# Optimization experiments

Hardware: AMD Instinct MI355X
Metric: run time of the kernel (lower is better)

The kernel has to match this reference:

```python
import jax, jax.numpy as jnp
import numpy as np

# ---- static config mirroring __init__ kwargs ----
B, GH, GW = 64, 52, 52
A, NC = 5, 80            # anchor_number, class_number
HW = GH * GW
MAXB = 30                # max_box_per_image
NET_W, NET_H = 416.0, 416.0
COORD_SCALE, NOOBJ_SCALE, OBJ_SCALE, CLASS_SCALE = 5.0, 1.0, 5.0, 1.0
OBJ_THRESH = 0.5
ANCHORS_NP = np.array([[10., 14.], [23., 27.], [37., 58.], [81., 82.], [135., 169.]], dtype=np.float32)


def setup_inputs() -> dict:
    key = jax.random.key(0)
    k1, k2, k3, k4, k5, k6, k7, k8 = jax.random.split(key, 8)
    net_out = jax.random.normal(k1, (B, GH, GW, A * (NC + 5)), jnp.float32) * 0.5
    # encoded targets [B, A, 6, HW]: (x_off, y_off, w_log, h_log, conf, class)
    xy = jax.random.uniform(k2, (B, A, 2, HW), jnp.float32)
    whlog = jax.random.normal(k3, (B, A, 2, HW), jnp.float32) * 0.3
    conf = jax.random.uniform(k4, (B, A, 1, HW), jnp.float32)
    cls = jnp.floor(jax.random.uniform(k5, (B, A, 1, HW), jnp.float32) * NC)
    targets = jnp.concatenate([xy, whlog, conf, cls], axis=2)
    anchor_mask = (jax.random.uniform(k6, (B, A, HW), jnp.float32) < 0.02).astype(jnp.float32)
    # GT boxes (x1,y1,x2,y2) in image pixels
    ctr = jax.random.uniform(k7, (B, MAXB, 2), jnp.float32) * NET_W
    sz = jax.random.uniform(k8, (B, MAXB, 2), jnp.float32) * 100.0 + 10.0
    true_bboxs = jnp.concatenate([ctr - sz / 2, ctr + sz / 2], axis=-1)
    anchors = jnp.asarray(ANCHORS_NP)
    return {"net_out": net_out, "targets": targets, "anchor_mask": anchor_mask,
            "true_bboxs": true_bboxs, "anchors": anchors}


def _focal(p, t, gamma=2.0):
    # F.binary_cross_entropy elementwise, then focal modulation
    bce = -(t * jnp.log(p) + (1.0 - t) * jnp.log1p(-p))
    pt = jnp.exp(-bce)
    return (1.0 - pt) ** gamma * bce


def reference(net_out, targets, anchor_mask, true_bboxs, anchors):
    Bs, gh, gw, _ = net_out.shape
    hw = gh * gw
    x = net_out.reshape(Bs, A, NC + 5, hw)
    xy = jax.nn.sigmoid(x[:, :, :2, :])          # [B,A,2,HW]
    wh = x[:, :, 2:4, :]                          # raw w,h logits
    p_conf = jax.nn.sigmoid(x[:, :, 4, :])       # [B,A,HW]

    # ----- class loss (CE over positives) -----
    clas = x[:, :, 5:, :].reshape(Bs * A, NC, hw).transpose(0, 2, 1).reshape(-1, NC)
    clas_mask = anchor_mask.reshape(Bs * A, 1, hw).transpose(0, 2, 1).reshape(-1)
    t_clas = targets[:, :, 5, :].reshape(Bs * A, 1, hw).transpose(0, 2, 1).reshape(-1).astype(jnp.int32)
    logp = jax.nn.log_softmax(clas, axis=-1)
    clas_loss = (-jnp.take_along_axis(logp, t_clas[:, None], axis=1)[:, 0]) * clas_mask

    # ----- coordinate loss (masked, size-weighted MSE) -----
    am = anchor_mask[:, :, None, :]  # [B,A,1,HW]
    wh_scale = 2.0 - targets[:, :, 2:3, :] * targets[:, :, 3:4, :] / (NET_W * NET_H)
    xy_loss = (xy - targets[:, :, 0:2, :]) ** 2 * am * wh_scale
    wh_loss = (wh - targets[:, :, 2:4, :]) ** 2 * am * wh_scale
    coords_loss = xy_loss.sum() + wh_loss.sum()

    # ----- rescale predictions to image-space corner boxes -----
    col = jnp.tile(jnp.arange(gw), gh).astype(jnp.float32)      # [HW]
    row = jnp.repeat(jnp.arange(gh), gw).astype(jnp.float32)    # [HW] (square grid)
    aw = anchors[:, 0][None, :, None]
    ah = anchors[:, 1][None, :, None]
    px = (xy[:, :, 0, :] + col) / gw * NET_W
    py = (xy[:, :, 1, :] + row) / gh * NET_H
    pw = jnp.exp(wh[:, :, 0, :]) * aw
    ph = jnp.exp(wh[:, :, 1, :]) * ah
    x1 = px - pw / 2
    y1 = py - ph / 2
    pred = jnp.stack([x1, y1, x1 + pw, y1 + ph], axis=-1)       # [B,A,HW,4]
    pred = pred.transpose(0, 2, 1, 3)[:, :, :, None, :]         # [B,HW,A,1,4]

    # ----- broadcast IoU vs GT boxes -----
    tb = true_bboxs[:, None, None, :, :]                         # [B,1,1,M,4]
    tl = jnp.maximum(pred[..., :2], tb[..., :2])
    br = jnp.minimum(pred[..., 2:], tb[..., 2:])
    whi = jnp.maximum(br - tl, 0.0)
    inter = whi[..., 0] * whi[..., 1]
    a1 = (pred[..., 2] - pred[..., 0]) * (pred[..., 3] - pred[..., 1])
    a2 = (tb[..., 2] - tb[..., 0]) * (tb[..., 3] - tb[..., 1])
    iou = inter / (a1 + a2 - inter + 1e-5)                       # [B,HW,A,M]
    iou_max = iou.max(axis=-1)                                   # [B,HW,A]

    noobj_mask = 1.0 - anchor_mask
    label_noobj = (iou_max < OBJ_THRESH).astype(jnp.float32).transpose(0, 2, 1) * noobj_mask

    # ----- focal confidence losses -----
    t_conf = targets[:, :, 4, :]
    fl = _focal(p_conf, t_conf)
    obj_conf_loss = (anchor_mask * fl).sum()
    noobj_conf_loss = (label_noobj * fl).sum()

    total = (clas_loss.sum() * CLASS_SCALE
             + coords_loss * COORD_SCALE
             + obj_conf_loss * OBJ_SCALE
             + noobj_conf_loss * NOOBJ_SCALE) / Bs
    return total
```

## Files before the change

kernel.cpp:

```cpp
#include <hip/hip_runtime.h>

#define BATCH   64
#define GH      52
#define GWID    52
#define HW      2704
#define NA      5
#define NC      80
#define MAXB    30
#define A_STRIDE  (85*HW)
#define NBA       (BATCH*NA)
#define GX_DENSE  3

__global__ __launch_bounds__(256) void yolo_main(
    const float* __restrict__ net_out,
    const float* __restrict__ targets,
    const float* __restrict__ amask,
    const float* __restrict__ tboxes,
    const float* __restrict__ anchors,
    float*       __restrict__ partial)
{
    __shared__ float tb[MAXB * 4];
    __shared__ float wred[4];

    const int ba   = blockIdx.y;
    const int b    = ba / NA;
    const int a    = ba - b * NA;
    const int tid  = threadIdx.x;
    const int lane = tid & 63;

    if (tid < MAXB * 4) tb[tid] = tboxes[(size_t)b * (MAXB * 4) + tid];
    __syncthreads();

    const int  p0    = (blockIdx.x * 256 + tid) * 4;
    const bool valid = (p0 < HW);
    const size_t nb    = (size_t)ba * A_STRIDE + (valid ? p0 : 0);
    const size_t tbase = (size_t)ba * 6 * HW   + (valid ? p0 : 0);

    float zx[4], zy[4], twp[4], thp[4], zc[4];
    float t_x[4], t_y[4], t_w[4], t_h[4], t_c[4], tcl[4], am[4];

    if (valid) {
        float4 v;
        v = *(const float4*)(net_out + nb);            zx[0]=v.x; zx[1]=v.y; zx[2]=v.z; zx[3]=v.w;
        v = *(const float4*)(net_out + nb + 1*HW);     zy[0]=v.x; zy[1]=v.y; zy[2]=v.z; zy[3]=v.w;
        v = *(const float4*)(net_out + nb + 2*HW);     twp[0]=v.x;twp[1]=v.y;twp[2]=v.z;twp[3]=v.w;
        v = *(const float4*)(net_out + nb + 3*HW);     thp[0]=v.x;thp[1]=v.y;thp[2]=v.z;thp[3]=v.w;
        v = *(const float4*)(net_out + nb + 4*HW);     zc[0]=v.x; zc[1]=v.y; zc[2]=v.z; zc[3]=v.w;
        v = *(const float4*)(targets + tbase);         t_x[0]=v.x;t_x[1]=v.y;t_x[2]=v.z;t_x[3]=v.w;
        v = *(const float4*)(targets + tbase + 1*HW);  t_y[0]=v.x;t_y[1]=v.y;t_y[2]=v.z;t_y[3]=v.w;
        v = *(const float4*)(targets + tbase + 2*HW);  t_w[0]=v.x;t_w[1]=v.y;t_w[2]=v.z;t_w[3]=v.w;
        v = *(const float4*)(targets + tbase + 3*HW);  t_h[0]=v.x;t_h[1]=v.y;t_h[2]=v.z;t_h[3]=v.w;
        v = *(const float4*)(targets + tbase + 4*HW);  t_c[0]=v.x;t_c[1]=v.y;t_c[2]=v.z;t_c[3]=v.w;
        v = *(const float4*)(targets + tbase + 5*HW);  tcl[0]=v.x;tcl[1]=v.y;tcl[2]=v.z;tcl[3]=v.w;
        v = *(const float4*)(amask + (size_t)ba * HW + p0); am[0]=v.x; am[1]=v.y; am[2]=v.z; am[3]=v.w;
    } else {
        #pragma unroll
        for (int j = 0; j < 4; ++j) {
            zx[j]=zy[j]=twp[j]=thp[j]=zc[j]=0.f;
            t_x[j]=t_y[j]=t_w[j]=t_h[j]=t_c[j]=tcl[j]=am[j]=0.f;
        }
    }

    const float aw = anchors[a * 2 + 0];
    const float ah = anchors[a * 2 + 1];

    float sx[4], sy[4], x1[4], y1[4], x2[4], y2[4], a1[4], io[4];
    #pragma unroll
    for (int j = 0; j < 4; ++j) {
        sx[j] = 1.f / (1.f + __builtin_expf(-zx[j]));
        sy[j] = 1.f / (1.f + __builtin_expf(-zy[j]));
        const int p = p0 + j;
        const float px = (sx[j] + (float)(p % GWID)) * (416.f / (float)GWID);
        const float py = (sy[j] + (float)(p / GWID)) * (416.f / (float)GH);
        const float pw = __builtin_expf(twp[j]) * aw;
        const float ph = __builtin_expf(thp[j]) * ah;
        x1[j] = px - pw * 0.5f;
        y1[j] = py - ph * 0.5f;
        x2[j] = x1[j] + pw;
        y2[j] = y1[j] + ph;
        a1[j] = pw * ph;
        io[j] = 0.f;
    }

    #pragma unroll
    for (int k = 0; k < MAXB; ++k) {
        const float bx1 = tb[k * 4 + 0];
        const float by1 = tb[k * 4 + 1];
        const float bx2 = tb[k * 4 + 2];
        const float by2 = tb[k * 4 + 3];
        const float a2  = (bx2 - bx1) * (by2 - by1);
        #pragma unroll
        for (int j = 0; j < 4; ++j) {
            const float wi = fmaxf(fminf(x2[j], bx2) - fmaxf(x1[j], bx1), 0.f);
            const float hi = fmaxf(fminf(y2[j], by2) - fmaxf(y1[j], by1), 0.f);
            const float inter = wi * hi;
            const float iou = inter / (a1[j] + a2 - inter + 1e-5f);
            io[j] = fmaxf(io[j], iou);
        }
    }

    float lsum = 0.f;
    #pragma unroll
    for (int j = 0; j < 4; ++j) {
        const float ws = 2.f - t_w[j] * t_h[j] * (1.f / (416.f * 416.f));
        const float dx = sx[j] - t_x[j], dy = sy[j] - t_y[j];
        const float dw = twp[j] - t_w[j], dh = thp[j] - t_h[j];
        const float coords = (dx*dx + dy*dy + dw*dw + dh*dh) * ws * am[j];

        const float log_pc   = -__builtin_logf(1.f + __builtin_expf(-zc[j]));
        const float log_1mpc = -__builtin_logf(1.f + __builtin_expf(zc[j]));
        const float bce = -(t_c[j] * log_pc + (1.f - t_c[j]) * log_1mpc);
        const float pt  = __builtin_expf(-bce);
        const float omp = 1.f - pt;
        const float fl  = omp * omp * bce;

        const float noobj = (io[j] < 0.5f) ? (1.f - am[j]) : 0.f;
        if (valid)
            lsum += 5.0f * coords + 5.0f * am[j] * fl + noobj * fl;
    }

    const size_t cbase = (size_t)ba * A_STRIDE + (size_t)5 * HW;
    #pragma unroll
    for (int j = 0; j < 4; ++j) {
        unsigned long long mb = __ballot(am[j] > 0.f);
        while (mb) {
            const int src = __ffsll((long long)mb) - 1;
            mb &= mb - 1;
            const int   p_s  = __shfl(p0, src, 64) + j;
            const float am_s = __shfl(am[j], src, 64);
            const int   tc_s = __shfl((int)tcl[j], src, 64);

            const size_t cb = cbase + p_s;
            const float v0 = net_out[cb + (size_t)lane * HW];
            const float v1 = (lane < (NC - 64))
                           ? net_out[cb + (size_t)(64 + lane) * HW]
                           : -1e30f;

            float mx = fmaxf(v0, v1);
            #pragma unroll
            for (int off = 32; off > 0; off >>= 1)
                mx = fmaxf(mx, __shfl_xor(mx, off, 64));

            float e = __builtin_expf(v0 - mx)
                    + ((lane < (NC - 64)) ? __builtin_expf(v1 - mx) : 0.f);
            #pragma unroll
            for (int off = 32; off > 0; off >>= 1)
                e += __shfl_xor(e, off, 64);

            const float vt = (tc_s < 64) ? __shfl(v0, tc_s, 64)
                                         : __shfl(v1, tc_s - 64, 64);

            if (lane == src)
                lsum += -(vt - mx - __builtin_logf(e)) * am_s;
        }
    }

    #pragma unroll
    for (int off = 32; off > 0; off >>= 1)
        lsum += __shfl_down(lsum, off, 64);
    const int wid = tid >> 6;
    if (lane == 0) wred[wid] = lsum;
    __syncthreads();
    if (tid == 0)
        partial[(size_t)blockIdx.y * GX_DENSE + blockIdx.x] =
            wred[0] + wred[1] + wred[2] + wred[3];
}

__global__ __launch_bounds__(256) void yolo_final(
    const float* __restrict__ partial, int n, float* __restrict__ out)
{
    __shared__ double sred[4];
    const int tid = threadIdx.x;
    double s = 0.0;
    for (int i = tid; i < n; i += 256) s += (double)partial[i];
    #pragma unroll
    for (int off = 32; off > 0; off >>= 1)
        s += __shfl_down(s, off, 64);
    const int wid  = tid >> 6;
    const int lane = tid & 63;
    if (lane == 0) sred[wid] = s;
    __syncthreads();
    if (tid == 0) {
        const double tot = sred[0] + sred[1] + sred[2] + sred[3];
        out[0] = (float)(tot / (double)BATCH);
    }
}

extern "C" void kernel_launch(void* const* d_in, const int* in_sizes, int n_in,
                              void* d_out, int out_size, void* d_ws, size_t ws_size,
                              hipStream_t stream) {
    const float* net_out = (const float*)d_in[0];
    const float* targets = (const float*)d_in[1];
    const float* amask   = (const float*)d_in[2];
    const float* tboxes  = (const float*)d_in[3];
    const float* anchors = (const float*)d_in[4];
    float* partial = (float*)d_ws;
    float* out = (float*)d_out;

    dim3 grid(GX_DENSE, NBA);
    yolo_main<<<grid, 256, 0, stream>>>(net_out, targets, amask, tboxes, anchors, partial);
    yolo_final<<<1, 256, 0, stream>>>(partial, GX_DENSE * NBA, out);
}
```

Before: 409.9 us.

## Split sparse class-loss into separate kernel with one position per thread

Moves the per-positive softmax cross-entropy out of the dense IoU/focal kernel into its own kernel, where each thread handles one grid position instead of four. The aim is to spread the serialized ballot loops over more waves and blocks and to lighten the dense kernel's register pressure and work. The cost is an extra launch, re-reading the anchor mask, and a larger final reduction.

Measured after the change: 411.1 us. About the same (+0.3%).

```diff
diff --git a/kernel.cpp b/kernel.cpp
--- a/kernel.cpp
+++ b/kernel.cpp
@@ -10,14 +10,15 @@
 #define A_STRIDE  (85*HW)
 #define NBA       (BATCH*NA)
 #define GX_DENSE  3
-
-__global__ __launch_bounds__(256) void yolo_main(
+#define GX_CLS    11
+
+__global__ __launch_bounds__(256) void yolo_dense(
     const float* __restrict__ net_out,
     const float* __restrict__ targets,
     const float* __restrict__ amask,
     const float* __restrict__ tboxes,
     const float* __restrict__ anchors,
-    float*       __restrict__ partial)
+    float*       __restrict__ partialA)
 {
     __shared__ float tb[MAXB * 4];
     __shared__ float wred[4];
@@ -37,7 +38,7 @@
     const size_t tbase = (size_t)ba * 6 * HW   + (valid ? p0 : 0);
 
     float zx[4], zy[4], twp[4], thp[4], zc[4];
-    float t_x[4], t_y[4], t_w[4], t_h[4], t_c[4], tcl[4], am[4];
+    float t_x[4], t_y[4], t_w[4], t_h[4], t_c[4], am[4];
 
     if (valid) {
         float4 v;
@@ -51,13 +52,12 @@
         v = *(const float4*)(targets + tbase + 2*HW);  t_w[0]=v.x;t_w[1]=v.y;t_w[2]=v.z;t_w[3]=v.w;
         v = *(const float4*)(targets + tbase + 3*HW);  t_h[0]=v.x;t_h[1]=v.y;t_h[2]=v.z;t_h[3]=v.w;
         v = *(const float4*)(targets + tbase + 4*HW);  t_c[0]=v.x;t_c[1]=v.y;t_c[2]=v.z;t_c[3]=v.w;
-        v = *(const float4*)(targets + tbase + 5*HW);  tcl[0]=v.x;tcl[1]=v.y;tcl[2]=v.z;tcl[3]=v.w;
         v = *(const float4*)(amask + (size_t)ba * HW + p0); am[0]=v.x; am[1]=v.y; am[2]=v.z; am[3]=v.w;
     } else {
         #pragma unroll
         for (int j = 0; j < 4; ++j) {
             zx[j]=zy[j]=twp[j]=thp[j]=zc[j]=0.f;
-            t_x[j]=t_y[j]=t_w[j]=t_h[j]=t_c[j]=tcl[j]=am[j]=0.f;
+            t_x[j]=t_y[j]=t_w[j]=t_h[j]=t_c[j]=am[j]=0.f;
         }
     }
 
@@ -119,42 +119,6 @@
             lsum += 5.0f * coords + 5.0f * am[j] * fl + noobj * fl;
     }
 
-    const size_t cbase = (size_t)ba * A_STRIDE + (size_t)5 * HW;
-    #pragma unroll
-    for (int j = 0; j < 4; ++j) {
-        unsigned long long mb = __ballot(am[j] > 0.f);
-        while (mb) {
-            const int src = __ffsll((long long)mb) - 1;
-            mb &= mb - 1;
-            const int   p_s  = __shfl(p0, src, 64) + j;
-            const float am_s = __shfl(am[j], src, 64);
-            const int   tc_s = __shfl((int)tcl[j], src, 64);
-
-            const size_t cb = cbase + p_s;
-            const float v0 = net_out[cb + (size_t)lane * HW];
-            const float v1 = (lane < (NC - 64))
-                           ? net_out[cb + (size_t)(64 + lane) * HW]
-                           : -1e30f;
-
-            float mx = fmaxf(v0, v1);
-            #pragma unroll
-            for (int off = 32; off > 0; off >>= 1)
-                mx = fmaxf(mx, __shfl_xor(mx, off, 64));
-
-            float e = __builtin_expf(v0 - mx)
-                    + ((lane < (NC - 64)) ? __builtin_expf(v1 - mx) : 0.f);
-            #pragma unroll
-            for (int off = 32; off > 0; off >>= 1)
-                e += __shfl_xor(e, off, 64);
-
-            const float vt = (tc_s < 64) ? __shfl(v0, tc_s, 64)
-                                         : __shfl(v1, tc_s - 64, 64);
-
-            if (lane == src)
-                lsum += -(vt - mx - __builtin_logf(e)) * am_s;
-        }
-    }
-
     #pragma unroll
     for (int off = 32; off > 0; off >>= 1)
         lsum += __shfl_down(lsum, off, 64);
@@ -162,17 +126,85 @@
     if (lane == 0) wred[wid] = lsum;
     __syncthreads();
     if (tid == 0)
-        partial[(size_t)blockIdx.y * GX_DENSE + blockIdx.x] =
+        partialA[(size_t)blockIdx.y * GX_DENSE + blockIdx.x] =
             wred[0] + wred[1] + wred[2] + wred[3];
 }
 
+__global__ __launch_bounds__(256) void yolo_class(
+    const float* __restrict__ net_out,
+    const float* __restrict__ targets,
+    const float* __restrict__ amask,
+    float*       __restrict__ partialB)
+{
+    __shared__ float wred[4];
+    const int ba   = blockIdx.y;
+    const int tid  = threadIdx.x;
+    const int lane = tid & 63;
+
+    const int  p_raw = blockIdx.x * 256 + tid;
+    const bool valid = (p_raw < HW);
+    const int  p     = valid ? p_raw : 0;
+
+    float am = valid ? amask[(size_t)ba * HW + p] : 0.f;
+    const int tcl = (am > 0.f)
+                  ? (int)targets[((size_t)ba * 6 + 5) * HW + p] : 0;
+
+    const size_t cbase = (size_t)ba * A_STRIDE + (size_t)5 * HW;
+    float lsum = 0.f;
+
+    unsigned long long mb = __ballot(am > 0.f);
+    while (mb) {
+        const int src = __ffsll((long long)mb) - 1;
+        mb &= mb - 1;
+        const int   p_s  = __shfl(p,   src, 64);
+        const float am_s = __shfl(am,  src, 64);
+        const int   tc_s = __shfl(tcl, src, 64);
+
+        const size_t cb = cbase + p_s;
+        const float v0 = net_out[cb + (size_t)lane * HW];
+        const float v1 = (lane < (NC - 64))
+                       ? net_out[cb + (size_t)(64 + lane) * HW]
+                       : -1e30f;
+
+        float mx = fmaxf(v0, v1);
+        #pragma unroll
+        for (int off = 32; off > 0; off >>= 1)
+            mx = fmaxf(mx, __shfl_xor(mx, off, 64));
+
+        float e = __builtin_expf(v0 - mx)
+                + ((lane < (NC - 64)) ? __builtin_expf(v1 - mx) : 0.f);
+        #pragma unroll
+        for (int off = 32; off > 0; off >>= 1)
+            e += __shfl_xor(e, off, 64);
+
+        const float vt = (tc_s < 64) ? __shfl(v0, tc_s, 64)
+                                     : __shfl(v1, tc_s - 64, 64);
+
+        if (lane == src)
+            lsum += -(vt - mx - __builtin_logf(e)) * am_s;
+    }
+
+    #pragma unroll
+    for (int off = 32; off > 0; off >>= 1)
+        lsum += __shfl_down(lsum, off, 64);
+    const int wid = tid >> 6;
+    if (lane == 0) wred[wid] = lsum;
+    __syncthreads();
+    if (tid == 0)
+        partialB[(size_t)blockIdx.y * GX_CLS + blockIdx.x] =
+            wred[0] + wred[1] + wred[2] + wred[3];
+}
+
 __global__ __launch_bounds__(256) void yolo_final(
-    const float* __restrict__ partial, int n, float* __restrict__ out)
+    const float* __restrict__ partialA, int nA,
+    const float* __restrict__ partialB, int nB,
+    float* __restrict__ out)
 {
     __shared__ double sred[4];
     const int tid = threadIdx.x;
     double s = 0.0;
-    for (int i = tid; i < n; i += 256) s += (double)partial[i];
+    for (int i = tid; i < nA; i += 256) s += (double)partialA[i];
+    for (int i = tid; i < nB; i += 256) s += (double)partialB[i];
     #pragma unroll
     for (int off = 32; off > 0; off >>= 1)
         s += __shfl_down(s, off, 64);
@@ -194,10 +226,14 @@
     const float* amask   = (const float*)d_in[2];
     const float* tboxes  = (const float*)d_in[3];
     const float* anchors = (const float*)d_in[4];
-    float* partial = (float*)d_ws;
-    float* out = (float*)d_out;
-
-    dim3 grid(GX_DENSE, NBA);
-    yolo_main<<<grid, 256, 0, stream>>>(net_out, targets, amask, tboxes, anchors, partial);
-    yolo_final<<<1, 256, 0, stream>>>(partial, GX_DENSE * NBA, out);
-}
+
+    float* partialA = (float*)d_ws;
+    float* partialB = (float*)d_ws + 4096;
+    float* out      = (float*)d_out;
+
+    dim3 gridA(GX_DENSE, NBA);
+    dim3 gridB(GX_CLS,   NBA);
+    yolo_dense<<<gridA, 256, 0, stream>>>(net_out, targets, amask, tboxes, anchors, partialA);
+    yolo_class<<<gridB, 256, 0, stream>>>(net_out, targets, amask, partialB);
+    yolo_final<<<1, 256, 0, stream>>>(partialA, GX_DENSE * NBA, partialB, GX_CLS * NBA, out);
+}
```
